# Optimization experiments

Hardware: AMD Instinct MI355X
Metric: run time of the kernel (lower is better)

The kernel has to match this reference:

```python
import jax, jax.numpy as jnp
import numpy as np
import math

B = 256          # batch size
D = 128          # input_size (embed dim)
N = 500000       # output_size == num_samples (memory bank rows)
K = 2048         # num_negative_samples
T = 0.07         # temperature
MOM = 0.5        # momentum
EPS = 1e-07


def _l2norm(x):
    return x / jnp.linalg.norm(x, axis=-1, keepdims=True)


def setup_inputs() -> dict:
    key = jax.random.key(0)
    k1, k2, k3, k4, k5, k6 = jax.random.split(key, 6)
    stdv = 1.0 / math.sqrt(D / 3.0)
    memory_v1 = jax.random.uniform(k1, (N, D), dtype=jnp.float32) * (2 * stdv) - stdv
    memory_v2 = jax.random.uniform(k2, (N, D), dtype=jnp.float32) * (2 * stdv) - stdv
    # embeds come out of an L2-normalization module in the original pipeline
    student_embed = _l2norm(jax.random.normal(k3, (B, D), dtype=jnp.float32))
    teacher_embed = _l2norm(jax.random.normal(k4, (B, D), dtype=jnp.float32))
    pos_idx = jax.random.randint(k5, (B,), 0, N, dtype=jnp.int64)
    contrast_idx = jax.random.randint(k6, (B, K + 1), 0, N, dtype=jnp.int64)
    contrast_idx = contrast_idx.at[:, 0].set(pos_idx)  # column 0 holds the positive
    return {
        'student_embed': student_embed,
        'teacher_embed': teacher_embed,
        'memory_v1': memory_v1,
        'memory_v2': memory_v2,
        'pos_idx': pos_idx,
        'contrast_idx': contrast_idx,
    }


def _contrast_loss(x):
    # x: [B, K+1] normalized exp-similarities; column 0 is the positive
    m = x.shape[1] - 1
    pn = 1.0 / float(N)  # num_samples
    noise = m * pn + EPS
    p_pos = x[:, 0]
    log_d1 = jnp.log(p_pos / (p_pos + noise))
    p_neg = x[:, 1:]
    log_d0 = jnp.log((m * pn) / (p_neg + noise))
    return -(log_d1.sum() + log_d0.sum()) / x.shape[0]


def reference(student_embed, teacher_embed, memory_v1, memory_v2, pos_idx, contrast_idx):
    output_size = memory_v1.shape[0]
    # gather [B, K+1, D] rows from each bank (detached in original)
    w1 = jax.lax.stop_gradient(memory_v1[contrast_idx])
    w2 = jax.lax.stop_gradient(memory_v2[contrast_idx])
    # per-sample bmm + exp/div  (teacher scored against v1 bank, student against v2)
    out_v2 = jnp.exp(jnp.einsum('bkd,bd->bk', w1, teacher_embed) / T)
    out_v1 = jnp.exp(jnp.einsum('bkd,bd->bk', w2, student_embed) / T)
    # first-call normalization constants (treated as constants thereafter)
    z_v1 = jax.lax.stop_gradient(out_v1.mean() * output_size)
    z_v2 = jax.lax.stop_gradient(out_v2.mean() * output_size)
    out_v1 = out_v1 / z_v1
    out_v2 = out_v2 / z_v2
    # momentum-weighted renormalize-and-scatter memory update (no_grad)
    s = jax.lax.stop_gradient(student_embed)
    t = jax.lax.stop_gradient(teacher_embed)
    l_pos = memory_v1[pos_idx] * MOM + s * (1.0 - MOM)
    updated_v1 = l_pos / jnp.sqrt((l_pos ** 2).sum(1, keepdims=True))
    new_memory_v1 = memory_v1.at[pos_idx].set(updated_v1)
    ab_pos = memory_v2[pos_idx] * MOM + t * (1.0 - MOM)
    updated_v2 = ab_pos / jnp.sqrt((ab_pos ** 2).sum(1, keepdims=True))
    new_memory_v2 = memory_v2.at[pos_idx].set(updated_v2)
    loss = _contrast_loss(out_v1) + _contrast_loss(out_v2)
    return loss, new_memory_v1, new_memory_v2
```

## Files before the change

kernel.cpp:

```cpp
#include <hip/hip_runtime.h>
#include <math.h>

namespace {
constexpr int kB = 256;
constexpr int kD = 128;
constexpr int kN = 500000;
constexpr int kKC = 2049;
constexpr int kNPair = kB * kKC;
constexpr float kTInv = 1.0f / 0.07f;
constexpr float kMom = 0.5f;
constexpr int kRB = 256;
constexpr long long kM = (long long)kN * kD;
constexpr long long kTot = 2 * kM;
}

__global__ __launch_bounds__(256) void dots_kernel(
    const float* __restrict__ mem1, const float* __restrict__ mem2,
    const float* __restrict__ teacher, const float* __restrict__ student,
    const int* __restrict__ cidx,
    float* __restrict__ e2, float* __restrict__ e1)
{
    int gtid = blockIdx.x * 256 + threadIdx.x;
    int wave = gtid >> 6;
    int lane = threadIdx.x & 63;
    if (wave >= kNPair) return;
    int b = wave / kKC;
    long long row = (long long)cidx[wave] * kD;
    const float2 m1 = *reinterpret_cast<const float2*>(mem1 + row + lane * 2);
    const float2 m2 = *reinterpret_cast<const float2*>(mem2 + row + lane * 2);
    const float2 tv = *reinterpret_cast<const float2*>(teacher + b * kD + lane * 2);
    const float2 sv = *reinterpret_cast<const float2*>(student + b * kD + lane * 2);
    float d1 = m1.x * tv.x + m1.y * tv.y;
    float d2 = m2.x * sv.x + m2.y * sv.y;
    #pragma unroll
    for (int off = 32; off > 0; off >>= 1) {
        d1 += __shfl_xor(d1, off);
        d2 += __shfl_xor(d2, off);
    }
    if (lane == 0) {
        e2[wave] = __expf(d1 * kTInv);
        e1[wave] = __expf(d2 * kTInv);
    }
}

__global__ __launch_bounds__(256) void sums_kernel(
    const float* __restrict__ e2, const float* __restrict__ e1,
    float* __restrict__ p2, float* __restrict__ p1)
{
    __shared__ float s2[256], s1[256];
    float a2 = 0.f, a1 = 0.f;
    for (int i = blockIdx.x * 256 + threadIdx.x; i < kNPair; i += 256 * kRB) {
        a2 += e2[i];
        a1 += e1[i];
    }
    s2[threadIdx.x] = a2; s1[threadIdx.x] = a1;
    __syncthreads();
    for (int st = 128; st > 0; st >>= 1) {
        if ((int)threadIdx.x < st) {
            s2[threadIdx.x] += s2[threadIdx.x + st];
            s1[threadIdx.x] += s1[threadIdx.x + st];
        }
        __syncthreads();
    }
    if (threadIdx.x == 0) { p2[blockIdx.x] = s2[0]; p1[blockIdx.x] = s1[0]; }
}

__global__ __launch_bounds__(256) void z_kernel(
    const float* __restrict__ p2, const float* __restrict__ p1, float* __restrict__ z)
{
    __shared__ float s2[256], s1[256];
    s2[threadIdx.x] = p2[threadIdx.x];
    s1[threadIdx.x] = p1[threadIdx.x];
    __syncthreads();
    for (int st = 128; st > 0; st >>= 1) {
        if ((int)threadIdx.x < st) {
            s2[threadIdx.x] += s2[threadIdx.x + st];
            s1[threadIdx.x] += s1[threadIdx.x + st];
        }
        __syncthreads();
    }
    if (threadIdx.x == 0) {
        const float scale = (float)kN / (float)kNPair;
        z[0] = s2[0] * scale;
        z[1] = s1[0] * scale;
    }
}

__global__ __launch_bounds__(256) void lossp_kernel(
    const float* __restrict__ e2, const float* __restrict__ e1,
    const float* __restrict__ z, float* __restrict__ lp)
{
    const float mpn = 2048.0f / 500000.0f;
    const float noise = mpn + 1e-7f;
    const float iz2 = 1.0f / z[0];
    const float iz1 = 1.0f / z[1];
    float acc = 0.f;
    for (int i = blockIdx.x * 256 + threadIdx.x; i < kNPair; i += 256 * kRB) {
        int k = i % kKC;
        float x2 = e2[i] * iz2;
        float x1 = e1[i] * iz1;
        if (k == 0) {
            acc += __logf(x2 / (x2 + noise)) + __logf(x1 / (x1 + noise));
        } else {
            acc += __logf(mpn / (x2 + noise)) + __logf(mpn / (x1 + noise));
        }
    }
    __shared__ float s[256];
    s[threadIdx.x] = acc;
    __syncthreads();
    for (int st = 128; st > 0; st >>= 1) {
        if ((int)threadIdx.x < st) s[threadIdx.x] += s[threadIdx.x + st];
        __syncthreads();
    }
    if (threadIdx.x == 0) lp[blockIdx.x] = s[0];
}

__global__ __launch_bounds__(256) void final_kernel(
    const float* __restrict__ lp, float* __restrict__ out)
{
    __shared__ float s[256];
    s[threadIdx.x] = lp[threadIdx.x];
    __syncthreads();
    for (int st = 128; st > 0; st >>= 1) {
        if ((int)threadIdx.x < st) s[threadIdx.x] += s[threadIdx.x + st];
        __syncthreads();
    }
    if (threadIdx.x == 0) out[0] = -s[0] / (float)kB;
}

__global__ __launch_bounds__(256) void copy_kernel(
    const float* __restrict__ mem1, const float* __restrict__ mem2,
    float* __restrict__ out)
{
    const long long NV4 = (kTot + 1) / 4;
    const long long KS  = kM / 4;
    const float4* m1v = reinterpret_cast<const float4*>(mem1);
    const float4* m2v = reinterpret_cast<const float4*>(mem2);
    float4* ov = reinterpret_cast<float4*>(out);
    long long stride = (long long)gridDim.x * 256;
    for (long long k = (long long)blockIdx.x * 256 + threadIdx.x; k < NV4; k += stride) {
        if (k == 0) {
            out[1] = mem1[0]; out[2] = mem1[1]; out[3] = mem1[2];
            out[kTot] = mem2[kM - 1];
            continue;
        }
        float4 r;
        if (k < KS) {
            float4 a = m1v[k - 1];
            float4 b = m1v[k];
            r = make_float4(a.w, b.x, b.y, b.z);
        } else if (k == KS) {
            r = make_float4(mem1[kM - 1], mem2[0], mem2[1], mem2[2]);
        } else {
            float4 a = m2v[k - KS - 1];
            float4 b = m2v[k - KS];
            r = make_float4(a.w, b.x, b.y, b.z);
        }
        ov[k] = r;
    }
}

__global__ __launch_bounds__(64) void update_kernel(
    const float* __restrict__ mem1, const float* __restrict__ mem2,
    const float* __restrict__ student, const float* __restrict__ teacher,
    const int* __restrict__ pos_idx,
    float* __restrict__ out1, float* __restrict__ out2)
{
    int b = blockIdx.x;
    int lane = threadIdx.x;
    int p = pos_idx[b];
    for (int b2 = b + 1; b2 < kB; ++b2)
        if (pos_idx[b2] == p) return;
    long long row = (long long)p * kD;
    float2 m1 = *reinterpret_cast<const float2*>(mem1 + row + lane * 2);
    float2 m2 = *reinterpret_cast<const float2*>(mem2 + row + lane * 2);
    float2 sv = *reinterpret_cast<const float2*>(student + b * kD + lane * 2);
    float2 tv = *reinterpret_cast<const float2*>(teacher + b * kD + lane * 2);
    float2 l1 = make_float2(m1.x * kMom + sv.x * (1.f - kMom),
                            m1.y * kMom + sv.y * (1.f - kMom));
    float2 l2 = make_float2(m2.x * kMom + tv.x * (1.f - kMom),
                            m2.y * kMom + tv.y * (1.f - kMom));
    float n1 = l1.x * l1.x + l1.y * l1.y;
    float n2 = l2.x * l2.x + l2.y * l2.y;
    #pragma unroll
    for (int off = 32; off > 0; off >>= 1) {
        n1 += __shfl_xor(n1, off);
        n2 += __shfl_xor(n2, off);
    }
    float i1 = 1.0f / sqrtf(n1);
    float i2 = 1.0f / sqrtf(n2);
    out1[row + lane * 2]     = l1.x * i1;
    out1[row + lane * 2 + 1] = l1.y * i1;
    out2[row + lane * 2]     = l2.x * i2;
    out2[row + lane * 2 + 1] = l2.y * i2;
}

extern "C" void kernel_launch(void* const* d_in, const int* in_sizes, int n_in,
                              void* d_out, int out_size, void* d_ws, size_t ws_size,
                              hipStream_t stream) {
    const float* student = (const float*)d_in[0];
    const float* teacher = (const float*)d_in[1];
    const float* mem1    = (const float*)d_in[2];
    const float* mem2    = (const float*)d_in[3];
    const int*   pos_idx = (const int*)d_in[4];
    const int*   cidx    = (const int*)d_in[5];

    float* out  = (float*)d_out;
    float* out1 = out + 1;
    float* out2 = out + 1 + kM;

    float* ws = (float*)d_ws;
    float* e2 = ws;
    float* e1 = ws + kNPair;
    float* p2 = e1 + kNPair;
    float* p1 = p2 + kRB;
    float* zz = p1 + kRB;
    float* lp = zz + 2;

    int nblocks = (kNPair + 3) / 4;
    dots_kernel<<<nblocks, 256, 0, stream>>>(mem1, mem2, teacher, student, cidx, e2, e1);
    sums_kernel<<<kRB, 256, 0, stream>>>(e2, e1, p2, p1);
    z_kernel<<<1, 256, 0, stream>>>(p2, p1, zz);
    lossp_kernel<<<kRB, 256, 0, stream>>>(e2, e1, zz, lp);
    final_kernel<<<1, 256, 0, stream>>>(lp, out);

    copy_kernel<<<2048, 256, 0, stream>>>(mem1, mem2, out);
    update_kernel<<<kB, 64, 0, stream>>>(mem1, mem2, student, teacher, pos_idx, out1, out2);
}
```

Before: 372.7 us.

## Bucket contrast indices by memory row and fuse dot products into bank copy

Builds a counting sort of the contrast indices by memory row (histogram, three-pass scan, atomic scatter), then runs one kernel that streams each memory row once. That kernel copies the row to the output and computes every dot product that references it, so the random gather of rows in a separate dots kernel goes away and the bank read is shared with the copy. In exchange it adds six extra launches, atomics over 500K counters, uncoalesced float2 copy stores, and a serial per-row loop with scattered e1/e2 writes. The old path is kept as a fallback when the workspace is too small.

```diff
diff --git a/kernel.cpp b/kernel.cpp
--- a/kernel.cpp
+++ b/kernel.cpp
@@ -12,7 +12,140 @@
 constexpr int kRB = 256;
 constexpr long long kM = (long long)kN * kD;
 constexpr long long kTot = 2 * kM;
-}
+constexpr int kChunk = 2048;
+constexpr int kNB1 = (kN + kChunk - 1) / kChunk;
+}
+
+
+__global__ __launch_bounds__(256) void zero2_kernel(int* __restrict__ A, int* __restrict__ cur)
+{
+    int i = blockIdx.x * 256 + threadIdx.x;
+    if (i < kN) { A[i] = 0; cur[i] = 0; }
+}
+
+__global__ __launch_bounds__(256) void hist_kernel(const int* __restrict__ cidx, int* __restrict__ A)
+{
+    int i = blockIdx.x * 256 + threadIdx.x;
+    if (i < kNPair) atomicAdd(&A[cidx[i]], 1);
+}
+
+__global__ __launch_bounds__(256) void scan1_kernel(const int* __restrict__ A, int* __restrict__ bsum)
+{
+    long long base = (long long)blockIdx.x * kChunk;
+    int t = threadIdx.x;
+    int s = 0;
+    #pragma unroll
+    for (int j = 0; j < 8; ++j) {
+        long long i = base + t * 8 + j;
+        if (i < kN) s += A[i];
+    }
+    __shared__ int lds[256];
+    lds[t] = s; __syncthreads();
+    for (int st = 128; st > 0; st >>= 1) {
+        if (t < st) lds[t] += lds[t + st];
+        __syncthreads();
+    }
+    if (t == 0) bsum[blockIdx.x] = lds[0];
+}
+
+__global__ __launch_bounds__(256) void scan2_kernel(
+    const int* __restrict__ bsum, int* __restrict__ bpre, int* __restrict__ offs)
+{
+    int t = threadIdx.x;
+    int v = (t < kNB1) ? bsum[t] : 0;
+    __shared__ int lds[256];
+    lds[t] = v; __syncthreads();
+    for (int st = 1; st < 256; st <<= 1) {
+        int add = (t >= st) ? lds[t - st] : 0;
+        __syncthreads();
+        lds[t] += add;
+        __syncthreads();
+    }
+    if (t < kNB1) bpre[t] = lds[t] - v;
+    if (t == kNB1 - 1) offs[kN] = lds[t];
+}
+
+__global__ __launch_bounds__(256) void scan3_kernel(
+    const int* __restrict__ A, const int* __restrict__ bpre, int* __restrict__ offs)
+{
+    int t = threadIdx.x;
+    long long base = (long long)blockIdx.x * kChunk;
+    int c[8]; int s = 0;
+    #pragma unroll
+    for (int j = 0; j < 8; ++j) {
+        long long i = base + t * 8 + j;
+        c[j] = (i < kN) ? A[i] : 0;
+        s += c[j];
+    }
+    __shared__ int lds[256];
+    lds[t] = s; __syncthreads();
+    for (int st = 1; st < 256; st <<= 1) {
+        int add = (t >= st) ? lds[t - st] : 0;
+        __syncthreads();
+        lds[t] += add;
+        __syncthreads();
+    }
+    int excl = lds[t] - s + bpre[blockIdx.x];
+    #pragma unroll
+    for (int j = 0; j < 8; ++j) {
+        long long i = base + t * 8 + j;
+        if (i < kN) { offs[i] = excl; excl += c[j]; }
+    }
+}
+
+__global__ __launch_bounds__(256) void scatter_kernel(
+    const int* __restrict__ cidx, const int* __restrict__ offs,
+    int* __restrict__ cur, int* __restrict__ sorted)
+{
+    int p = blockIdx.x * 256 + threadIdx.x;
+    if (p < kNPair) {
+        int r = cidx[p];
+        int pos = offs[r] + atomicAdd(&cur[r], 1);
+        sorted[pos] = p;
+    }
+}
+
+__global__ __launch_bounds__(256) void fused_kernel(
+    const float* __restrict__ mem1, const float* __restrict__ mem2,
+    const float* __restrict__ teacher, const float* __restrict__ student,
+    const int* __restrict__ offs, const int* __restrict__ sorted,
+    float* __restrict__ out, float* __restrict__ e2, float* __restrict__ e1)
+{
+    int lane = threadIdx.x & 63;
+    int wid  = (blockIdx.x * 256 + threadIdx.x) >> 6;
+    int nw   = (gridDim.x * 256) >> 6;
+    for (int r = wid; r < kN; r += nw) {
+        long long rb = (long long)r * kD;
+        float2 a = *reinterpret_cast<const float2*>(mem1 + rb + lane * 2);
+        float2 b = *reinterpret_cast<const float2*>(mem2 + rb + lane * 2);
+        float* o1 = out + 1 + rb;
+        float* o2 = out + 1 + kM + rb;
+        o1[lane * 2]     = a.x;
+        o1[lane * 2 + 1] = a.y;
+        o2[lane * 2]     = b.x;
+        o2[lane * 2 + 1] = b.y;
+        int off = offs[r];
+        int cnt = offs[r + 1] - off;
+        for (int i = 0; i < cnt; ++i) {
+            int p  = sorted[off + i];
+            int bb = p / kKC;
+            const float2 tv = *reinterpret_cast<const float2*>(teacher + bb * kD + lane * 2);
+            const float2 sv = *reinterpret_cast<const float2*>(student + bb * kD + lane * 2);
+            float d1 = a.x * tv.x + a.y * tv.y;
+            float d2 = b.x * sv.x + b.y * sv.y;
+            #pragma unroll
+            for (int o = 32; o > 0; o >>= 1) {
+                d1 += __shfl_xor(d1, o);
+                d2 += __shfl_xor(d2, o);
+            }
+            if (lane == 0) {
+                e2[p] = __expf(d1 * kTInv);
+                e1[p] = __expf(d2 * kTInv);
+            }
+        }
+    }
+}
+
 
 __global__ __launch_bounds__(256) void dots_kernel(
     const float* __restrict__ mem1, const float* __restrict__ mem2,
@@ -42,6 +175,39 @@
         e1[wave] = __expf(d2 * kTInv);
     }
 }
+
+__global__ __launch_bounds__(256) void copy_kernel(
+    const float* __restrict__ mem1, const float* __restrict__ mem2,
+    float* __restrict__ out)
+{
+    const long long NV4 = (kTot + 1) / 4;
+    const long long KS  = kM / 4;
+    const float4* m1v = reinterpret_cast<const float4*>(mem1);
+    const float4* m2v = reinterpret_cast<const float4*>(mem2);
+    float4* ov = reinterpret_cast<float4*>(out);
+    long long stride = (long long)gridDim.x * 256;
+    for (long long k = (long long)blockIdx.x * 256 + threadIdx.x; k < NV4; k += stride) {
+        if (k == 0) {
+            out[1] = mem1[0]; out[2] = mem1[1]; out[3] = mem1[2];
+            out[kTot] = mem2[kM - 1];
+            continue;
+        }
+        float4 r;
+        if (k < KS) {
+            float4 a = m1v[k - 1];
+            float4 b = m1v[k];
+            r = make_float4(a.w, b.x, b.y, b.z);
+        } else if (k == KS) {
+            r = make_float4(mem1[kM - 1], mem2[0], mem2[1], mem2[2]);
+        } else {
+            float4 a = m2v[k - KS - 1];
+            float4 b = m2v[k - KS];
+            r = make_float4(a.w, b.x, b.y, b.z);
+        }
+        ov[k] = r;
+    }
+}
+
 
 __global__ __launch_bounds__(256) void sums_kernel(
     const float* __restrict__ e2, const float* __restrict__ e1,
@@ -128,37 +294,6 @@
     if (threadIdx.x == 0) out[0] = -s[0] / (float)kB;
 }
 
-__global__ __launch_bounds__(256) void copy_kernel(
-    const float* __restrict__ mem1, const float* __restrict__ mem2,
-    float* __restrict__ out)
-{
-    const long long NV4 = (kTot + 1) / 4;
-    const long long KS  = kM / 4;
-    const float4* m1v = reinterpret_cast<const float4*>(mem1);
-    const float4* m2v = reinterpret_cast<const float4*>(mem2);
-    float4* ov = reinterpret_cast<float4*>(out);
-    long long stride = (long long)gridDim.x * 256;
-    for (long long k = (long long)blockIdx.x * 256 + threadIdx.x; k < NV4; k += stride) {
-        if (k == 0) {
-            out[1] = mem1[0]; out[2] = mem1[1]; out[3] = mem1[2];
-            out[kTot] = mem2[kM - 1];
-            continue;
-        }
-        float4 r;
-        if (k < KS) {
-            float4 a = m1v[k - 1];
-            float4 b = m1v[k];
-            r = make_float4(a.w, b.x, b.y, b.z);
-        } else if (k == KS) {
-            r = make_float4(mem1[kM - 1], mem2[0], mem2[1], mem2[2]);
-        } else {
-            float4 a = m2v[k - KS - 1];
-            float4 b = m2v[k - KS];
-            r = make_float4(a.w, b.x, b.y, b.z);
-        }
-        ov[k] = r;
-    }
-}
 
 __global__ __launch_bounds__(64) void update_kernel(
     const float* __restrict__ mem1, const float* __restrict__ mem2,
@@ -211,19 +346,37 @@
 
     float* ws = (float*)d_ws;
     float* e2 = ws;
-    float* e1 = ws + kNPair;
+    float* e1 = e2 + kNPair;
     float* p2 = e1 + kNPair;
     float* p1 = p2 + kRB;
     float* zz = p1 + kRB;
     float* lp = zz + 2;
-
-    int nblocks = (kNPair + 3) / 4;
-    dots_kernel<<<nblocks, 256, 0, stream>>>(mem1, mem2, teacher, student, cidx, e2, e1);
+    int*   A      = (int*)(lp + kRB);
+    int*   cur    = A + kN;
+    int*   offs   = cur + kN;
+    int*   bsum   = offs + kN + 1;
+    int*   bpre   = bsum + kNB1;
+    int*   sorted = bpre + kNB1;
+    size_t need = (size_t)((char*)(sorted + kNPair) - (char*)d_ws);
+
+    if (ws_size >= need) {
+        zero2_kernel<<<(kN + 255) / 256, 256, 0, stream>>>(A, cur);
+        hist_kernel<<<(kNPair + 255) / 256, 256, 0, stream>>>(cidx, A);
+        scan1_kernel<<<kNB1, 256, 0, stream>>>(A, bsum);
+        scan2_kernel<<<1, 256, 0, stream>>>(bsum, bpre, offs);
+        scan3_kernel<<<kNB1, 256, 0, stream>>>(A, bpre, offs);
+        scatter_kernel<<<(kNPair + 255) / 256, 256, 0, stream>>>(cidx, offs, cur, sorted);
+        fused_kernel<<<2048, 256, 0, stream>>>(mem1, mem2, teacher, student,
+                                               offs, sorted, out, e2, e1);
+    } else {
+        int nblocks = (kNPair + 3) / 4;
+        dots_kernel<<<nblocks, 256, 0, stream>>>(mem1, mem2, teacher, student, cidx, e2, e1);
+        copy_kernel<<<2048, 256, 0, stream>>>(mem1, mem2, out);
+    }
+
     sums_kernel<<<kRB, 256, 0, stream>>>(e2, e1, p2, p1);
     z_kernel<<<1, 256, 0, stream>>>(p2, p1, zz);
     lossp_kernel<<<kRB, 256, 0, stream>>>(e2, e1, zz, lp);
     final_kernel<<<1, 256, 0, stream>>>(lp, out);
-
-    copy_kernel<<<2048, 256, 0, stream>>>(mem1, mem2, out);
     update_kernel<<<kB, 64, 0, stream>>>(mem1, mem2, student, teacher, pos_idx, out1, out2);
 }
```

New measurement: 397.3 us. 1.07x slower.

## Fuse bank copy and gather-dot kernels into one block-partitioned persistent kernel

Applied to the files above, without the earlier changes.

Merges the memory-bank copy and the gathered dot-product/exp kernels into one launch, with 5/8 of the blocks doing the streaming copy and 3/8 running a persistent grid-stride dot loop. The bandwidth-bound copy and the latency-bound random gathers can then overlap instead of running back to back. The dot path now uses half-waves with float4 loads, one half per bank, and prefetches the next row and index ahead of use. The fixed block split may leave one side idle once the other finishes.

```diff
diff --git a/kernel.cpp b/kernel.cpp
--- a/kernel.cpp
+++ b/kernel.cpp
@@ -12,36 +12,87 @@
 constexpr int kRB = 256;
 constexpr long long kM = (long long)kN * kD;
 constexpr long long kTot = 2 * kM;
-}
-
-__global__ __launch_bounds__(256) void dots_kernel(
+constexpr int kBlocks = 2048;
+constexpr int kCopyBlocks = kBlocks / 8 * 5;
+constexpr int kDotsBlocks = kBlocks / 8 * 3;
+constexpr long long kCopyThreads = (long long)kCopyBlocks * 256;
+constexpr long long kDotsWaves = (long long)kDotsBlocks * 4;
+}
+
+__global__ __launch_bounds__(256) void mixed_kernel(
     const float* __restrict__ mem1, const float* __restrict__ mem2,
     const float* __restrict__ teacher, const float* __restrict__ student,
     const int* __restrict__ cidx,
-    float* __restrict__ e2, float* __restrict__ e1)
-{
-    int gtid = blockIdx.x * 256 + threadIdx.x;
-    int wave = gtid >> 6;
-    int lane = threadIdx.x & 63;
-    if (wave >= kNPair) return;
-    int b = wave / kKC;
-    long long row = (long long)cidx[wave] * kD;
-    const float2 m1 = *reinterpret_cast<const float2*>(mem1 + row + lane * 2);
-    const float2 m2 = *reinterpret_cast<const float2*>(mem2 + row + lane * 2);
-    const float2 tv = *reinterpret_cast<const float2*>(teacher + b * kD + lane * 2);
-    const float2 sv = *reinterpret_cast<const float2*>(student + b * kD + lane * 2);
-    float d1 = m1.x * tv.x + m1.y * tv.y;
-    float d2 = m2.x * sv.x + m2.y * sv.y;
-    #pragma unroll
-    for (int off = 32; off > 0; off >>= 1) {
-        d1 += __shfl_xor(d1, off);
-        d2 += __shfl_xor(d2, off);
-    }
-    if (lane == 0) {
-        e2[wave] = __expf(d1 * kTInv);
-        e1[wave] = __expf(d2 * kTInv);
-    }
-}
+    float* __restrict__ out, float* __restrict__ e2, float* __restrict__ e1)
+{
+    const int grp = blockIdx.x & 7;
+    if (grp < 5) {
+        const long long NV4 = (kTot + 1) / 4;
+        const long long KS  = kM / 4;
+        const float4* m1v = reinterpret_cast<const float4*>(mem1);
+        const float4* m2v = reinterpret_cast<const float4*>(mem2);
+        float4* ov = reinterpret_cast<float4*>(out);
+        long long copyRank = (long long)(blockIdx.x >> 3) * 5 + grp;
+        for (long long k = copyRank * 256 + threadIdx.x; k < NV4; k += kCopyThreads) {
+            if (k == 0) {
+                out[1] = mem1[0]; out[2] = mem1[1]; out[3] = mem1[2];
+                out[kTot] = mem2[kM - 1];
+                continue;
+            }
+            float4 r;
+            if (k < KS) {
+                float4 a = m1v[k - 1];
+                float4 b = m1v[k];
+                r = make_float4(a.w, b.x, b.y, b.z);
+            } else if (k == KS) {
+                r = make_float4(mem1[kM - 1], mem2[0], mem2[1], mem2[2]);
+            } else {
+                float4 a = m2v[k - KS - 1];
+                float4 b = m2v[k - KS];
+                r = make_float4(a.w, b.x, b.y, b.z);
+            }
+            ov[k] = r;
+        }
+    } else {
+        const int lane = threadIdx.x & 63;
+        const int half = lane >> 5;
+        const int c = lane & 31;
+        const float4* bank4 = reinterpret_cast<const float4*>(half ? mem2 : mem1);
+        const float4* emb4  = reinterpret_cast<const float4*>(half ? student : teacher);
+        float* ep = half ? e1 : e2;
+
+        long long dotsRank = (long long)(blockIdx.x >> 3) * 3 + (grp - 5);
+        long long wid = dotsRank * 4 + (threadIdx.x >> 6);
+
+        long long p0 = wid;
+        if (p0 >= kNPair) return;
+        int r0 = cidx[p0];
+        float4 rv = bank4[(long long)r0 * 32 + c];
+        float4 ev = emb4[(long long)((unsigned)p0 / (unsigned)kKC) * 32 + c];
+        int rn = (p0 + kDotsWaves < kNPair) ? cidx[p0 + kDotsWaves] : 0;
+
+        for (long long p = p0; p < kNPair; p += kDotsWaves) {
+            long long pn  = p + kDotsWaves;
+            long long pn2 = p + 2 * kDotsWaves;
+            int rn2 = (pn2 < kNPair) ? cidx[pn2] : 0;
+            float4 rvn = make_float4(0.f, 0.f, 0.f, 0.f);
+            float4 evn = rvn;
+            if (pn < kNPair) {
+                rvn = bank4[(long long)rn * 32 + c];
+                evn = emb4[(long long)((unsigned)pn / (unsigned)kKC) * 32 + c];
+            }
+            float d = rv.x * ev.x + rv.y * ev.y + rv.z * ev.z + rv.w * ev.w;
+            d += __shfl_xor(d, 16);
+            d += __shfl_xor(d, 8);
+            d += __shfl_xor(d, 4);
+            d += __shfl_xor(d, 2);
+            d += __shfl_xor(d, 1);
+            if (c == 0) ep[p] = __expf(d * kTInv);
+            rv = rvn; ev = evn; rn = rn2;
+        }
+    }
+}
+
 
 __global__ __launch_bounds__(256) void sums_kernel(
     const float* __restrict__ e2, const float* __restrict__ e1,
@@ -128,37 +179,6 @@
     if (threadIdx.x == 0) out[0] = -s[0] / (float)kB;
 }
 
-__global__ __launch_bounds__(256) void copy_kernel(
-    const float* __restrict__ mem1, const float* __restrict__ mem2,
-    float* __restrict__ out)
-{
-    const long long NV4 = (kTot + 1) / 4;
-    const long long KS  = kM / 4;
-    const float4* m1v = reinterpret_cast<const float4*>(mem1);
-    const float4* m2v = reinterpret_cast<const float4*>(mem2);
-    float4* ov = reinterpret_cast<float4*>(out);
-    long long stride = (long long)gridDim.x * 256;
-    for (long long k = (long long)blockIdx.x * 256 + threadIdx.x; k < NV4; k += stride) {
-        if (k == 0) {
-            out[1] = mem1[0]; out[2] = mem1[1]; out[3] = mem1[2];
-            out[kTot] = mem2[kM - 1];
-            continue;
-        }
-        float4 r;
-        if (k < KS) {
-            float4 a = m1v[k - 1];
-            float4 b = m1v[k];
-            r = make_float4(a.w, b.x, b.y, b.z);
-        } else if (k == KS) {
-            r = make_float4(mem1[kM - 1], mem2[0], mem2[1], mem2[2]);
-        } else {
-            float4 a = m2v[k - KS - 1];
-            float4 b = m2v[k - KS];
-            r = make_float4(a.w, b.x, b.y, b.z);
-        }
-        ov[k] = r;
-    }
-}
 
 __global__ __launch_bounds__(64) void update_kernel(
     const float* __restrict__ mem1, const float* __restrict__ mem2,
@@ -211,19 +231,17 @@
 
     float* ws = (float*)d_ws;
     float* e2 = ws;
-    float* e1 = ws + kNPair;
+    float* e1 = e2 + kNPair;
     float* p2 = e1 + kNPair;
     float* p1 = p2 + kRB;
     float* zz = p1 + kRB;
     float* lp = zz + 2;
 
-    int nblocks = (kNPair + 3) / 4;
-    dots_kernel<<<nblocks, 256, 0, stream>>>(mem1, mem2, teacher, student, cidx, e2, e1);
+    mixed_kernel<<<kBlocks, 256, 0, stream>>>(mem1, mem2, teacher, student,
+                                              cidx, out, e2, e1);
     sums_kernel<<<kRB, 256, 0, stream>>>(e2, e1, p2, p1);
     z_kernel<<<1, 256, 0, stream>>>(p2, p1, zz);
     lossp_kernel<<<kRB, 256, 0, stream>>>(e2, e1, zz, lp);
     final_kernel<<<1, 256, 0, stream>>>(lp, out);
-
-    copy_kernel<<<2048, 256, 0, stream>>>(mem1, mem2, out);
     update_kernel<<<kB, 64, 0, stream>>>(mem1, mem2, student, teacher, pos_idx, out1, out2);
 }
```

Result: slower. 385.9 us (+3.5%).
